# Kernel tuning notes

Measured on AMD Instinct MI355X. Metric: run time of the kernel, lower is better.

Reference implementation:

```python
import jax, jax.numpy as jnp
import numpy as np

K = 20          # cfg.K, k-NN neighbors
NEG = 0.2       # LeakyReLU slope
EPS = 1e-5      # BatchNorm eps (eval mode, running mean=0, var=1)
BN_SCALE = np.float32(1.0 / np.sqrt(1.0 + EPS))


def graph_feature(x, k):
    # x: [B, C, N] -> [B, 2C, N, k] (DGCNN get_graph_feature)
    xt = jnp.swapaxes(x, 1, 2)                                  # [B,N,C]
    xx = jnp.sum(xt * xt, axis=-1)                              # [B,N]
    inner = jnp.einsum('bnc,bmc->bnm', xt, xt)
    negdist = 2.0 * inner - xx[:, :, None] - xx[:, None, :]     # -||xi-xj||^2
    _, idx = jax.lax.top_k(negdist, k)                          # [B,N,k]
    feat = jax.vmap(lambda xb, ib: xb[ib])(xt, idx)             # [B,N,k,C]
    center = jnp.broadcast_to(xt[:, :, None, :], feat.shape)
    out = jnp.concatenate([feat - center, center], axis=-1)     # [B,N,k,2C]
    return jnp.transpose(out, (0, 3, 1, 2))


def edge_layer(x, W, b, g, beta):
    # 1x1 Conv2d + BN(eval) + LeakyReLU + max over k
    f = graph_feature(x, K)                                     # [B,2C,N,k]
    y = jnp.einsum('oc,bcnk->bonk', W, f) + b[:, None, None]
    y = y * (g[:, None, None] * BN_SCALE) + beta[:, None, None]
    y = jnp.where(y >= 0, y, NEG * y)
    return jnp.max(y, axis=-1)                                  # [B,O,N]


def edge_conv(x, Ws, bs, gs, betas):
    for W, b, g, beta in zip(Ws, bs, gs, betas):
        x = edge_layer(x, W, b, g, beta)
    return x


def mha(x, Wi, bi, Wo, bo, nh=8):
    # torch nn.MultiheadAttention(64, 8, batch_first=True), self-attention
    B, N, E = x.shape
    d = E // nh
    qkv = x @ Wi.T + bi
    q, k_, v = jnp.split(qkv, 3, axis=-1)
    hd = lambda t: jnp.transpose(t.reshape(B, N, nh, d), (0, 2, 1, 3))
    q, k_, v = hd(q), hd(k_), hd(v)
    a = jax.nn.softmax(jnp.einsum('bhnd,bhmd->bhnm', q, k_) / np.float32(np.sqrt(d)), axis=-1)
    o = jnp.einsum('bhnm,bhmd->bhnd', a, v)
    o = jnp.transpose(o, (0, 2, 1, 3)).reshape(B, N, E)
    return o @ Wo.T + bo


def branch(feats, cW, cb, cg, cB, sW, sb, sg, sB, Wi, bi, Wo, bo):
    xyz = feats[:, 0:3, :]
    sem = feats[:, 3:, :]
    xyz = edge_conv(xyz, cW, cb, cg, cB)                         # [B,32,N]
    sem = edge_conv(sem, sW, sb, sg, sB)                         # [B,32,N]
    fuse = jnp.concatenate([jnp.swapaxes(xyz, 1, 2), jnp.swapaxes(sem, 1, 2)], axis=2)  # [B,N,64]
    fuse = mha(fuse, Wi, bi, Wo, bo)
    B, N, E = fuse.shape
    return fuse.reshape(B, N, E // 2, 2).mean(axis=-1)           # AvgPool1d(2,2) -> [B,N,32]


def attention_pool(emb, W):
    # SimGNN-style attention readout
    g = jnp.tanh(jnp.mean(emb @ W, axis=1))                      # [B,F]
    scores = jax.nn.sigmoid(jnp.einsum('bnf,bf->bn', emb, g))    # [B,N]
    pooled = jnp.einsum('bnf,bn->bf', emb, scores)               # [B,F]
    return pooled, scores[..., None]


def setup_inputs() -> dict:
    key = jax.random.key(0)
    ks = iter(jax.random.split(key, 48))
    nrm = lambda shape, s=0.05: jax.random.normal(next(ks), shape, dtype=jnp.float32) * s
    B, N = 8, 1024
    inp = {
        'features_1': jax.random.normal(next(ks), (B, 15, N), jnp.float32),
        'features_2': jax.random.normal(next(ks), (B, 15, N), jnp.float32),
    }
    dims_c = [(64, 6), (128, 128), (32, 256)]    # center_conv (in=3)
    dims_s = [(64, 24), (128, 128), (32, 256)]   # sem_conv (in=12)
    for pre, dims in (('c', dims_c), ('s', dims_s)):
        for i, (o, c) in enumerate(dims):
            inp[pre + 'w%d' % i] = nrm((o, c))
            inp[pre + 'b%d' % i] = jnp.zeros((o,), jnp.float32)
            inp[pre + 'g%d' % i] = jnp.ones((o,), jnp.float32)
            inp[pre + 'B%d' % i] = jnp.zeros((o,), jnp.float32)
    inp['mha_wi'] = nrm((192, 64)); inp['mha_bi'] = jnp.zeros((192,), jnp.float32)
    inp['mha_wo'] = nrm((64, 64));  inp['mha_bo'] = jnp.zeros((64,), jnp.float32)
    inp['att_w'] = nrm((32, 32), 0.1)
    inp['ntn_w'] = nrm((32, 32, 16)); inp['ntn_v'] = nrm((16, 32)); inp['ntn_b'] = jnp.zeros((16,), jnp.float32)
    inp['fc1_w'] = nrm((16, 16)); inp['fc1_b'] = jnp.zeros((16,), jnp.float32)
    inp['sc_w'] = nrm((1, 16));  inp['sc_b'] = jnp.zeros((1,), jnp.float32)
    return inp


def reference(features_1, features_2,
              cw0, cb0, cg0, cB0, cw1, cb1, cg1, cB1, cw2, cb2, cg2, cB2,
              sw0, sb0, sg0, sB0, sw1, sb1, sg1, sB1, sw2, sb2, sg2, sB2,
              mha_wi, mha_bi, mha_wo, mha_bo,
              att_w, ntn_w, ntn_v, ntn_b, fc1_w, fc1_b, sc_w, sc_b):
    cW, cb, cg, cB = [cw0, cw1, cw2], [cb0, cb1, cb2], [cg0, cg1, cg2], [cB0, cB1, cB2]
    sW, sb, sg, sB = [sw0, sw1, sw2], [sb0, sb1, sb2], [sg0, sg1, sg2], [sB0, sB1, sB2]
    a1 = branch(features_1, cW, cb, cg, cB, sW, sb, sg, sB, mha_wi, mha_bi, mha_wo, mha_bo)
    a2 = branch(features_2, cW, cb, cg, cB, sW, sb, sg, sB, mha_wi, mha_bi, mha_wo, mha_bo)
    p1, s1 = attention_pool(a1, att_w)
    p2, s2 = attention_pool(a2, att_w)
    d = p1 - p2                                                  # [B,32]
    t = jax.nn.relu(jnp.einsum('bf,fgt,bg->bt', d, ntn_w, d) + d @ ntn_v.T + ntn_b)  # [B,16]
    h = jax.nn.relu(t @ fc1_w.T + fc1_b)
    score = jax.nn.sigmoid(h @ sc_w.T + sc_b).reshape(-1)        # [B]
    return score, s1, s2
```

## Files before the change

### kernel.cpp

```cpp
#include <hip/hip_runtime.h>
#include <math.h>

#define BD 16
#define ND 1024
#define KNN 20
#define NEGS 0.2f
#define BNSC 0.99999500003749969482f
#define KSL 8
#define KPS 128

__device__ __forceinline__ float leakyf(float y){ return y >= 0.f ? y : NEGS*y; }

__device__ __forceinline__ void gl_lds16(const float* g, float* l){
  __builtin_amdgcn_global_load_lds(
      (const __attribute__((address_space(1))) void*)g,
      (__attribute__((address_space(3))) void*)l, 16, 0, 0);
}


template<int C, int CS>
__global__ __launch_bounds__(256) void k_prep(const float* __restrict__ f1,
                                              const float* __restrict__ f2,
                                              float* __restrict__ x,
                                              float* __restrict__ xx, int c0){
  int blk = blockIdx.x;
  int b = blk & 15;
  int n = (blk >> 4)*256 + threadIdx.x;
  const float* feat = (b & 8) ? f2 : f1;
  int b8 = b & 7;
  float v[CS];
  float s = 0.f;
  #pragma unroll
  for (int c = 0; c < C; ++c){
    v[c] = feat[((size_t)(b8*15) + c0 + c)*ND + n];
    s = fmaf(v[c], v[c], s);
  }
  #pragma unroll
  for (int c = C; c < CS; ++c) v[c] = 0.f;
  #pragma unroll
  for (int g = 0; g < CS/4; ++g)
    *(float4*)&x[(size_t)(b*CS + g*4)*ND + (size_t)n*4] =
        make_float4(v[g*4], v[g*4+1], v[g*4+2], v[g*4+3]);
  xx[b*ND + n] = s;
}

__global__ __launch_bounds__(256)
void k_knn(const float* __restrict__ x,
    const float* __restrict__ xx, int* __restrict__ idxp, int CS, int nchunk){
  __shared__ __align__(16) float Xc[2][2][4096];
  int b = blockIdx.x & 15;
  int r0 = (blockIdx.x >> 4)*16;
  int t = threadIdx.x;
  int lane = t & 63;
  int w = __builtin_amdgcn_readfirstlane(t >> 6);
  const float* xb = x + (size_t)b*ND*CS;
  float acc[4][16];
  #pragma unroll
  for (int j = 0; j < 4; ++j)
    #pragma unroll
    for (int q = 0; q < 16; ++q) acc[j][q] = 0.f;

  auto stage = [&](int buf, int ch){
    int g0 = 2*ch, g1 = 2*ch + 1;
    bool v1 = (g1*4 < CS);
    #pragma unroll
    for (int i = 0; i < 4; ++i){
      int m = i*256 + t;
      unsigned ub = (unsigned)((i*256 + (w << 6))*4);
      gl_lds16(&xb[((size_t)g0*ND + m)*4], &Xc[buf][0][ub]);
      if (v1) gl_lds16(&xb[((size_t)g1*ND + m)*4], &Xc[buf][1][ub]);
      else    *(float4*)&Xc[buf][1][m*4] = make_float4(0.f,0.f,0.f,0.f);
    }
  };

  stage(0, 0);
  __syncthreads();
  int cur = 0;
  for (int ch = 0; ch < nchunk; ++ch){
    bool more = (ch + 1 < nchunk);
    if (more) stage(cur ^ 1, ch + 1);
    float4 rv0[4], rv1[4];
    #pragma unroll
    for (int j = 0; j < 4; ++j){
      rv0[j] = *(const float4*)&Xc[cur][0][(r0 + w*4 + j)*4];
      rv1[j] = *(const float4*)&Xc[cur][1][(r0 + w*4 + j)*4];
    }
    #pragma unroll
    for (int q = 0; q < 16; ++q){
      float4 cv0 = *(const float4*)&Xc[cur][0][(q*64 + lane)*4];
      float4 cv1 = *(const float4*)&Xc[cur][1][(q*64 + lane)*4];
      #pragma unroll
      for (int j = 0; j < 4; ++j){
        float s = acc[j][q];
        s = fmaf(rv0[j].x, cv0.x, s); s = fmaf(rv0[j].y, cv0.y, s);
        s = fmaf(rv0[j].z, cv0.z, s); s = fmaf(rv0[j].w, cv0.w, s);
        s = fmaf(rv1[j].x, cv1.x, s); s = fmaf(rv1[j].y, cv1.y, s);
        s = fmaf(rv1[j].z, cv1.z, s); s = fmaf(rv1[j].w, cv1.w, s);
        acc[j][q] = s;
      }
    }
    if (more){
      __syncthreads();
      cur ^= 1;
    }
  }
  float xxm[16];
  #pragma unroll
  for (int q = 0; q < 16; ++q) xxm[q] = xx[b*ND + q*64 + lane];
  unsigned uk[4][16];
  #pragma unroll
  for (int j = 0; j < 4; ++j){
    float xr = xx[b*ND + r0 + w*4 + j];
    #pragma unroll
    for (int q = 0; q < 16; ++q){
      float f = 2.f*acc[j][q] - xr - xxm[q];
      unsigned bv = __float_as_uint(f);
      uk[j][q] = (bv & 0x80000000u) ? ~bv : (bv | 0x80000000u);
    }
  }
  unsigned pref[4] = {0u, 0u, 0u, 0u};
  unsigned done = 0u;
  #pragma unroll 1
  for (int bit = 30; bit >= 0; --bit){
    #pragma unroll
    for (int u = 0; u < 4; ++u){
      if (done & (1u << u)) continue;
      unsigned cand = pref[u] | (1u << bit);
      int c = 0;
      #pragma unroll
      for (int q = 0; q < 16; ++q)
        c += (int)__popcll(__ballot(uk[u][q] >= cand));
      if (c >= KNN){
        pref[u] = cand;
        if (c == KNN) done |= (1u << u);
      }
    }
    if (done == 15u) break;
  }
  unsigned long long mlt = (1ull << lane) - 1ull;
  #pragma unroll
  for (int u = 0; u < 4; ++u){
    unsigned T = pref[u];
    int cg = 0;
    #pragma unroll
    for (int q = 0; q < 16; ++q) cg += (int)__popcll(__ballot(uk[u][q] > T));
    int need_eq = KNN - cg;
    int* op = &idxp[((size_t)(b*ND + r0 + w*4 + u))*KNN];
    int run_gt = 0, run_eq = 0;
    #pragma unroll
    for (int q = 0; q < 16; ++q){
      unsigned k = uk[u][q];
      unsigned long long bg = __ballot(k > T);
      unsigned long long be = __ballot(k == T);
      if (k > T) op[run_gt + (int)__popcll(bg & mlt)] = q*64 + lane;
      if (k == T){
        int r = run_eq + (int)__popcll(be & mlt);
        if (r < need_eq) op[cg + r] = q*64 + lane;
      }
      run_gt += (int)__popcll(bg);
      run_eq += (int)__popcll(be);
    }
  }
}

template<int O>
__global__ __launch_bounds__(256) void k_phaseA(const float* __restrict__ x,
    const float* __restrict__ W, const float* __restrict__ bias,
    const float* __restrict__ gamma, const float* __restrict__ beta,
    float* __restrict__ zs, float* __restrict__ ccv, int C, int XS){
  constexpr int TO = O/16;
  constexpr int WP = O + 4;
  __shared__ float W1s[32*WP];
  __shared__ float dWs[32*WP];
  __shared__ float Xs[32*33];
  int blk = blockIdx.x;
  int b = blk & 15, n0 = (blk >> 4)*32;
  int t = threadIdx.x;
  int ot = t & 15, nt = t >> 4;
  int obase = ot*TO;
  int nl = nt*2;
  float az[TO][2] = {}, ac[TO][2] = {};
  for (int cc = 0; cc < C; cc += 32){
    int KC = (C - cc < 32) ? (C - cc) : 32;
    int NG = (KC + 3) >> 2;
    for (int i = t; i < O*KC; i += 256){
      int o = i % O, c = i / O;
      float w1 = W[(size_t)o*2*C + cc + c];
      float w2 = W[(size_t)o*2*C + C + cc + c];
      W1s[c*WP + o] = w1;
      dWs[c*WP + o] = w2 - w1;
    }
    for (int i = t; i < 32*NG; i += 256){
      int row = i & 31, g = i >> 5;
      float4 v = *(const float4*)&x[(size_t)(b*XS + cc + g*4)*ND + (size_t)(n0+row)*4];
      Xs[(g*4+0)*33 + row] = v.x;
      Xs[(g*4+1)*33 + row] = v.y;
      Xs[(g*4+2)*33 + row] = v.z;
      Xs[(g*4+3)*33 + row] = v.w;
    }
    __syncthreads();
    for (int c = 0; c < KC; ++c){
      float xv0 = Xs[c*33 + nl];
      float xv1 = Xs[c*33 + nl + 1];
      #pragma unroll
      for (int i = 0; i < TO; ++i){
        float w1 = W1s[c*WP + obase + i];
        float dw = dWs[c*WP + obase + i];
        az[i][0] = fmaf(w1, xv0, az[i][0]);
        az[i][1] = fmaf(w1, xv1, az[i][1]);
        ac[i][0] = fmaf(dw, xv0, ac[i][0]);
        ac[i][1] = fmaf(dw, xv1, ac[i][1]);
      }
    }
    __syncthreads();
  }
  #pragma unroll
  for (int i = 0; i < TO; ++i){
    int o = obase + i;
    float alpha = gamma[o]*BNSC;
    float bb = bias[o], be = beta[o];
    #pragma unroll
    for (int q = 0; q < 2; ++q){
      int n = n0 + nl + q;
      size_t off = ((size_t)b*ND + n)*O + o;
      zs[off]  = az[i][q]*alpha;
      ccv[off] = fmaf(ac[i][q] + bb, alpha, be);
    }
  }
}

template<bool DOXX, bool TILED>
__global__ __launch_bounds__(256) void k_phaseB(const float* __restrict__ zs,
    const float* __restrict__ ccv, const int* __restrict__ idxp,
    float* __restrict__ outp, float* __restrict__ xxout,
    int O, int ostride, int ooff){
  int t = threadIdx.x;
  int lane = t & 63, w = t >> 6;
  int b = blockIdx.x & 15;
  int n = (blockIdx.x >> 4)*4 + w;
  int gn = (b << 10) + n;
  int mm[KNN];
  const int* ip = idxp + (size_t)gn*KNN;
  #pragma unroll
  for (int k = 0; k < KNN; ++k) mm[k] = ip[k];
  float sq = 0.f;
  for (int o = lane; o < O; o += 64){
    float cvv = ccv[(size_t)gn*O + o];
    float mx = -INFINITY;
    #pragma unroll 4
    for (int k = 0; k < KNN; ++k){
      float v = leakyf(zs[((size_t)(b*ND) + mm[k])*O + o] + cvv);
      mx = fmaxf(mx, v);
    }
    if (TILED)
      outp[(size_t)(b*O + (o & ~3))*ND + (size_t)n*4 + (o & 3)] = mx;
    else
      outp[(size_t)gn*ostride + ooff + o] = mx;
    if (DOXX) sq = fmaf(mx, mx, sq);
  }
  if (DOXX){
    #pragma unroll
    for (int off = 32; off; off >>= 1) sq += __shfl_down(sq, off);
    if (lane == 0) xxout[gn] = sq;
  }
}

__global__ __launch_bounds__(256) void k_lin(const float* __restrict__ in,
    const float* __restrict__ Wm, const float* __restrict__ bias,
    float* __restrict__ outp){
  int b = blockIdx.x & 15;
  int inner = (blockIdx.x >> 4)*256 + threadIdx.x;
  int o = inner % 192; int n = inner / 192;
  int bn = (b << 10) + n;
  const float4* ip = (const float4*)(in + (size_t)bn*64);
  const float4* wp = (const float4*)(Wm + (size_t)o*64);
  float s = bias[o];
  #pragma unroll
  for (int c = 0; c < 16; ++c){
    float4 a = ip[c], wv = wp[c];
    s = fmaf(a.x, wv.x, s); s = fmaf(a.y, wv.y, s);
    s = fmaf(a.z, wv.z, s); s = fmaf(a.w, wv.w, s);
  }
  outp[(size_t)bn*192 + o] = s;
}

__global__ __launch_bounds__(256, 1) void k_attn_part(const float* __restrict__ qkv,
    float* __restrict__ pl, float* __restrict__ pacc){
  __shared__ __align__(16) float Ks[2][KPS*8];
  __shared__ __align__(16) float Vs[2][KPS*8];
  int blk = blockIdx.x;
  int b = blk & 15; int ksl = (blk >> 4) & 7; int hp = blk >> 7;
  int t = threadIdx.x;
  int hh = t >> 7;
  int h = hp*2 + hh;
  int lq = t & 127;
  for (int i = t; i < 2*KPS*8; i += 256){
    int hi = (i >= KPS*8) ? 1 : 0;
    int r = i - hi*KPS*8;
    int m = r >> 3, dd = r & 7;
    size_t base = ((size_t)b*ND + ksl*KPS + m)*192 + (hp*2 + hi)*8 + dd;
    Ks[hi][r] = qkv[base + 64];
    Vs[hi][r] = qkv[base + 128];
  }
  __syncthreads();
  const float scale = 0.35355339059327373f;
  float q[8][8];
  #pragma unroll
  for (int u = 0; u < 8; ++u){
    int n = u*128 + lq;
    const float4* qp = (const float4*)(qkv + ((size_t)b*ND + n)*192 + h*8);
    float4 q0 = qp[0], q1 = qp[1];
    q[u][0]=q0.x*scale; q[u][1]=q0.y*scale; q[u][2]=q0.z*scale; q[u][3]=q0.w*scale;
    q[u][4]=q1.x*scale; q[u][5]=q1.y*scale; q[u][6]=q1.z*scale; q[u][7]=q1.w*scale;
  }
  float l[8] = {};
  float acc[8][8] = {};
  for (int m = 0; m < KPS; ++m){
    float4 k0 = *(const float4*)&Ks[hh][m*8];
    float4 k1 = *(const float4*)&Ks[hh][m*8+4];
    float4 v0 = *(const float4*)&Vs[hh][m*8];
    float4 v1 = *(const float4*)&Vs[hh][m*8+4];
    #pragma unroll
    for (int u = 0; u < 8; ++u){
      float s;
      s = q[u][0]*k0.x;           s = fmaf(q[u][1], k0.y, s);
      s = fmaf(q[u][2], k0.z, s); s = fmaf(q[u][3], k0.w, s);
      s = fmaf(q[u][4], k1.x, s); s = fmaf(q[u][5], k1.y, s);
      s = fmaf(q[u][6], k1.z, s); s = fmaf(q[u][7], k1.w, s);
      float p = __expf(s);
      l[u] += p;
      acc[u][0] = fmaf(p, v0.x, acc[u][0]);
      acc[u][1] = fmaf(p, v0.y, acc[u][1]);
      acc[u][2] = fmaf(p, v0.z, acc[u][2]);
      acc[u][3] = fmaf(p, v0.w, acc[u][3]);
      acc[u][4] = fmaf(p, v1.x, acc[u][4]);
      acc[u][5] = fmaf(p, v1.y, acc[u][5]);
      acc[u][6] = fmaf(p, v1.z, acc[u][6]);
      acc[u][7] = fmaf(p, v1.w, acc[u][7]);
    }
  }
  #pragma unroll
  for (int u = 0; u < 8; ++u){
    int n = u*128 + lq;
    size_t pidx = (((size_t)(b*8 + h))*8 + ksl)*ND + n;
    pl[pidx] = l[u];
    float4* ap = (float4*)&pacc[pidx*8];
    ap[0] = make_float4(acc[u][0], acc[u][1], acc[u][2], acc[u][3]);
    ap[1] = make_float4(acc[u][4], acc[u][5], acc[u][6], acc[u][7]);
  }
}

__global__ __launch_bounds__(256) void k_attn_comb(const float* __restrict__ pl,
    const float* __restrict__ pacc, float* __restrict__ attno){
  int b = blockIdx.x & 15;
  int inner = (blockIdx.x >> 4)*256 + threadIdx.x;
  int h = inner >> 10; int n = inner & 1023;
  int bh = b*8 + h;
  float L = 0.f;
  float o[8] = {};
  #pragma unroll
  for (int s = 0; s < KSL; ++s){
    size_t pidx = ((size_t)bh*8 + s)*ND + n;
    L += pl[pidx];
    const float4* ap = (const float4*)&pacc[pidx*8];
    float4 a0 = ap[0], a1 = ap[1];
    o[0] += a0.x; o[1] += a0.y; o[2] += a0.z; o[3] += a0.w;
    o[4] += a1.x; o[5] += a1.y; o[6] += a1.z; o[7] += a1.w;
  }
  float inv = 1.f/L;
  float4* dst = (float4*)&attno[((size_t)b*ND + n)*64 + h*8];
  dst[0] = make_float4(o[0]*inv, o[1]*inv, o[2]*inv, o[3]*inv);
  dst[1] = make_float4(o[4]*inv, o[5]*inv, o[6]*inv, o[7]*inv);
}

__global__ __launch_bounds__(256) void k_projmean(const float* __restrict__ attno,
    const float* __restrict__ Wo, const float* __restrict__ bo,
    float* __restrict__ emb){
  int b = blockIdx.x & 15;
  int inner = (blockIdx.x >> 4)*256 + threadIdx.x;
  int n = inner >> 5; int f = inner & 31;
  int bn = (b << 10) + n;
  const float4* ip = (const float4*)(attno + (size_t)bn*64);
  int o0 = 2*f, o1 = 2*f + 1;
  const float4* w0 = (const float4*)(Wo + (size_t)o0*64);
  const float4* w1 = (const float4*)(Wo + (size_t)o1*64);
  float s0 = bo[o0], s1 = bo[o1];
  #pragma unroll
  for (int c = 0; c < 16; ++c){
    float4 a = ip[c], u = w0[c], v = w1[c];
    s0 = fmaf(a.x,u.x,s0); s0 = fmaf(a.y,u.y,s0); s0 = fmaf(a.z,u.z,s0); s0 = fmaf(a.w,u.w,s0);
    s1 = fmaf(a.x,v.x,s1); s1 = fmaf(a.y,v.y,s1); s1 = fmaf(a.z,v.z,s1); s1 = fmaf(a.w,v.w,s1);
  }
  emb[(size_t)bn*32 + f] = 0.5f*(s0 + s1);
}

__global__ __launch_bounds__(256) void k_poolfuse(const float* __restrict__ emb,
    const float* __restrict__ attw, float* __restrict__ sout,
    float* __restrict__ pooled){
  __shared__ float part[8][32];
  __shared__ float meanv[32];
  __shared__ float gv[32];
  __shared__ float sc[ND];
  int b = blockIdx.x, t = threadIdx.x;
  int f = t & 31, j = t >> 5;
  const float* eb = emb + (size_t)b*ND*32;
  float s = 0.f;
  for (int n = j; n < ND; n += 8) s += eb[n*32 + f];
  part[j][f] = s;
  __syncthreads();
  if (t < 32){
    float m = 0.f;
    for (int j2 = 0; j2 < 8; ++j2) m += part[j2][t];
    meanv[t] = m * (1.f/ND);
  }
  __syncthreads();
  if (t < 32){
    float acc = 0.f;
    for (int f2 = 0; f2 < 32; ++f2) acc = fmaf(meanv[f2], attw[f2*32 + t], acc);
    gv[t] = tanhf(acc);
  }
  __syncthreads();
  for (int n = t; n < ND; n += 256){
    const float4* ep = (const float4*)(eb + n*32);
    float acc = 0.f;
    #pragma unroll
    for (int f4 = 0; f4 < 8; ++f4){
      float4 e = ep[f4];
      acc = fmaf(e.x, gv[f4*4+0], acc);
      acc = fmaf(e.y, gv[f4*4+1], acc);
      acc = fmaf(e.z, gv[f4*4+2], acc);
      acc = fmaf(e.w, gv[f4*4+3], acc);
    }
    float sg = 1.f/(1.f + __expf(-acc));
    sout[(size_t)b*ND + n] = sg;
    sc[n] = sg;
  }
  __syncthreads();
  float pacc = 0.f;
  for (int n = j; n < ND; n += 8) pacc = fmaf(eb[n*32 + f], sc[n], pacc);
  part[j][f] = pacc;
  __syncthreads();
  if (t < 32){
    float m = 0.f;
    for (int j2 = 0; j2 < 8; ++j2) m += part[j2][t];
    pooled[b*32 + t] = m;
  }
}

__global__ __launch_bounds__(256) void k_head(const float* __restrict__ p1,
    const float* __restrict__ p2, const float* __restrict__ ntnw,
    const float* __restrict__ ntnv, const float* __restrict__ ntnb,
    const float* __restrict__ fc1w, const float* __restrict__ fc1b,
    const float* __restrict__ scw, const float* __restrict__ scb,
    float* __restrict__ outscore){
  __shared__ __align__(16) float Wl[8192];
  __shared__ float Vl[512];
  __shared__ float F1[256];
  __shared__ float ds[8][32];
  __shared__ float tv[8][16];
  __shared__ float hv[8][16];
  int t = threadIdx.x;
  {
    int b = t >> 5, f = t & 31;
    ds[b][f] = p1[b*32+f] - p2[b*32+f];
  }
  for (int i = t; i < 512; i += 256) Vl[i] = ntnv[i];
  if (t < 256) F1[t] = fc1w[t];
  float acc = 0.f;
  for (int ph = 0; ph < 2; ++ph){
    __syncthreads();
    {
      const float4* src = (const float4*)(ntnw + ph*8192);
      float4* dst = (float4*)Wl;
      for (int i = t; i < 2048; i += 256) dst[i] = src[i];
    }
    __syncthreads();
    if (t < 128){
      int b = t >> 4, tt = t & 15;
      for (int fi = 0; fi < 16; ++fi){
        float df = ds[b][ph*16 + fi];
        #pragma unroll 8
        for (int gg = 0; gg < 32; ++gg)
          acc = fmaf(df*ds[b][gg], Wl[(fi*32+gg)*16 + tt], acc);
      }
    }
  }
  if (t < 128){
    int b = t >> 4, tt = t & 15;
    acc += ntnb[tt];
    for (int gg = 0; gg < 32; ++gg) acc = fmaf(ds[b][gg], Vl[tt*32+gg], acc);
    tv[b][tt] = fmaxf(acc, 0.f);
  }
  __syncthreads();
  if (t < 128){
    int b = t >> 4, i = t & 15;
    float a2 = fc1b[i];
    for (int kk = 0; kk < 16; ++kk) a2 = fmaf(tv[b][kk], F1[i*16+kk], a2);
    hv[b][i] = fmaxf(a2, 0.f);
  }
  __syncthreads();
  if (t < 8){
    float a3 = scb[0];
    for (int i = 0; i < 16; ++i) a3 = fmaf(hv[t][i], scw[i], a3);
    outscore[t] = 1.f/(1.f + __expf(-a3));
  }
}

extern "C" void kernel_launch(void* const* d_in, const int* in_sizes, int n_in,
                              void* d_out, int out_size, void* d_ws, size_t ws_size,
                              hipStream_t stream) {
  auto F = [&](int i){ return (const float*)d_in[i]; };
  const float* f1 = F(0); const float* f2 = F(1);
  const float* cw[3] = { F(2), F(6), F(10) };
  const float* cb[3] = { F(3), F(7), F(11) };
  const float* cg[3] = { F(4), F(8), F(12) };
  const float* cB[3] = { F(5), F(9), F(13) };
  const float* sw[3] = { F(14), F(18), F(22) };
  const float* sb[3] = { F(15), F(19), F(23) };
  const float* sg[3] = { F(16), F(20), F(24) };
  const float* sB[3] = { F(17), F(21), F(25) };
  const float* mha_wi = F(26); const float* mha_bi = F(27);
  const float* mha_wo = F(28); const float* mha_bo = F(29);
  const float* att_w  = F(30);
  const float* ntn_w  = F(31); const float* ntn_v = F(32); const float* ntn_b = F(33);
  const float* fc1_w  = F(34); const float* fc1_b = F(35);
  const float* sc_w   = F(36); const float* sc_b  = F(37);
  float* out = (float*)d_out;

  char* ws = (char*)d_ws;
  const size_t MB = 1 << 20;
  float* xA   = (float*)(ws + 0*MB);
  float* xB   = (float*)(ws + 8*MB);
  float* zs   = (float*)(ws + 16*MB);
  float* cvb  = (float*)(ws + 24*MB);
  int*   idxb = (int*)  (ws + 32*MB);
  float* xxb  = (float*)(ws + 34*MB);
  float* fuse = (float*)(ws + 35*MB);
  float* qkv   = (float*)(ws + 0*MB);
  float* plb   = (float*)(ws + 12*MB);
  float* paccb = (float*)(ws + 16*MB);
  float* attno = (float*)(ws + 48*MB);
  float* emb   = (float*)(ws + 52*MB);
  float* pooled= (float*)(ws + 54*MB);
  (void)ws_size;

  auto knn = [&](const float* xin, int CS, int nch8){
    k_knn<<<BD*64, 256, 0, stream>>>(xin, xxb, idxb, CS, nch8);
  };
  auto phA = [&](const float* xin, int C, int XS, int O, const float* W, const float* bb,
                 const float* gg, const float* be){
    if (O == 64)       k_phaseA<64> <<<BD*32, 256, 0, stream>>>(xin, W, bb, gg, be, zs, cvb, C, XS);
    else if (O == 128) k_phaseA<128><<<BD*32, 256, 0, stream>>>(xin, W, bb, gg, be, zs, cvb, C, XS);
    else               k_phaseA<32> <<<BD*32, 256, 0, stream>>>(xin, W, bb, gg, be, zs, cvb, C, XS);
  };

  for (int part = 0; part < 2; ++part){
    const float* const* Wl = part ? sw : cw;
    const float* const* bl = part ? sb : cb;
    const float* const* gl = part ? sg : cg;
    const float* const* Bl = part ? sB : cB;
    int C0 = part ? 12 : 3;
    int CS0 = part ? 12 : 4;
    if (part) k_prep<12,12><<<BD*ND/256, 256, 0, stream>>>(f1, f2, xA, xxb, 3);
    else      k_prep<3, 4> <<<BD*ND/256, 256, 0, stream>>>(f1, f2, xA, xxb, 0);
    knn(xA, CS0, part ? 2 : 1);
    phA(xA, C0, CS0, 64, Wl[0], bl[0], gl[0], Bl[0]);
    k_phaseB<true,true><<<BD*ND/4, 256, 0, stream>>>(zs, cvb, idxb, xB, xxb, 64, 0, 0);
    knn(xB, 64, 8);
    phA(xB, 64, 64, 128, Wl[1], bl[1], gl[1], Bl[1]);
    k_phaseB<true,true><<<BD*ND/4, 256, 0, stream>>>(zs, cvb, idxb, xA, xxb, 128, 0, 0);
    knn(xA, 128, 16);
    phA(xA, 128, 128, 32, Wl[2], bl[2], gl[2], Bl[2]);
    k_phaseB<false,false><<<BD*ND/4, 256, 0, stream>>>(zs, cvb, idxb, fuse, nullptr, 32, 64, part*32);
  }
  k_lin<<<(BD*ND*192)/256, 256, 0, stream>>>(fuse, mha_wi, mha_bi, qkv);
  k_attn_part<<<BD*4*KSL, 256, 0, stream>>>(qkv, plb, paccb);
  k_attn_comb<<<(BD*8*ND)/256, 256, 0, stream>>>(plb, paccb, attno);
  k_projmean<<<(BD*ND*32)/256, 256, 0, stream>>>(attno, mha_wo, mha_bo, emb);
  k_poolfuse<<<BD, 256, 0, stream>>>(emb, att_w, out + 8, pooled);
  k_head<<<1, 256, 0, stream>>>(pooled, pooled + 256, ntn_w, ntn_v, ntn_b,
                                fc1_w, fc1_b, sc_w, sc_b, out);
}
```

Baseline: 1.103 ms.

## Register-tile the QKV input projection with LDS-staged weights and inputs

Rewrites k_lin as a tiled GEMM. Each block stages the full transposed 192x64 weight matrix and a 32-row input tile in LDS, and each thread computes a 12x2 output micro-tile with float4 stores. This replaces one-output-per-thread dot products that reread input and weights from global memory. In exchange, every block reloads about 48KB of weights, which raises LDS usage, lowers occupancy, and adds bank conflicts on the transposed weight writes.

```diff
diff --git a/kernel.cpp b/kernel.cpp
--- a/kernel.cpp
+++ b/kernel.cpp
@@ -268,20 +268,52 @@
 __global__ __launch_bounds__(256) void k_lin(const float* __restrict__ in,
     const float* __restrict__ Wm, const float* __restrict__ bias,
     float* __restrict__ outp){
-  int b = blockIdx.x & 15;
-  int inner = (blockIdx.x >> 4)*256 + threadIdx.x;
-  int o = inner % 192; int n = inner / 192;
-  int bn = (b << 10) + n;
-  const float4* ip = (const float4*)(in + (size_t)bn*64);
-  const float4* wp = (const float4*)(Wm + (size_t)o*64);
-  float s = bias[o];
-  #pragma unroll
-  for (int c = 0; c < 16; ++c){
-    float4 a = ip[c], wv = wp[c];
-    s = fmaf(a.x, wv.x, s); s = fmaf(a.y, wv.y, s);
-    s = fmaf(a.z, wv.z, s); s = fmaf(a.w, wv.w, s);
-  }
-  outp[(size_t)bn*192 + o] = s;
+  __shared__ float Ws[64*196];
+  __shared__ float Xs[64*33];
+  int blk = blockIdx.x;
+  int b = blk & 15, n0 = (blk >> 4)*32;
+  int bn0 = (b << 10) + n0;
+  int t = threadIdx.x;
+  int ot = t & 15, nt = t >> 4;
+  int obase = ot*12;
+  int nl = nt*2;
+  for (int i = t; i < 192*64; i += 256){
+    int c = i & 63, o = i >> 6;
+    Ws[c*196 + o] = Wm[i];
+  }
+  for (int i = t; i < 32*16; i += 256){
+    int row = i >> 4, c4 = i & 15;
+    float4 v = *(const float4*)&in[((size_t)(bn0 + row))*64 + c4*4];
+    Xs[(c4*4+0)*33 + row] = v.x;
+    Xs[(c4*4+1)*33 + row] = v.y;
+    Xs[(c4*4+2)*33 + row] = v.z;
+    Xs[(c4*4+3)*33 + row] = v.w;
+  }
+  __syncthreads();
+  float acc[12][2];
+  #pragma unroll
+  for (int i = 0; i < 12; ++i){
+    float bb = bias[obase + i];
+    acc[i][0] = bb; acc[i][1] = bb;
+  }
+  for (int c = 0; c < 64; ++c){
+    float xv0 = Xs[c*33 + nl];
+    float xv1 = Xs[c*33 + nl + 1];
+    #pragma unroll
+    for (int i = 0; i < 12; ++i){
+      float wv = Ws[c*196 + obase + i];
+      acc[i][0] = fmaf(wv, xv0, acc[i][0]);
+      acc[i][1] = fmaf(wv, xv1, acc[i][1]);
+    }
+  }
+  #pragma unroll
+  for (int q = 0; q < 2; ++q){
+    float* op = &outp[(size_t)(bn0 + nl + q)*192 + obase];
+    #pragma unroll
+    for (int v4 = 0; v4 < 3; ++v4)
+      *(float4*)&op[v4*4] = make_float4(acc[v4*4+0][q], acc[v4*4+1][q],
+                                        acc[v4*4+2][q], acc[v4*4+3][q]);
+  }
 }
 
 __global__ __launch_bounds__(256, 1) void k_attn_part(const float* __restrict__ qkv,
@@ -573,7 +605,7 @@
     phA(xA, 128, 128, 32, Wl[2], bl[2], gl[2], Bl[2]);
     k_phaseB<false,false><<<BD*ND/4, 256, 0, stream>>>(zs, cvb, idxb, fuse, nullptr, 32, 64, part*32);
   }
-  k_lin<<<(BD*ND*192)/256, 256, 0, stream>>>(fuse, mha_wi, mha_bi, qkv);
+  k_lin<<<BD*32, 256, 0, stream>>>(fuse, mha_wi, mha_bi, qkv);
   k_attn_part<<<BD*4*KSL, 256, 0, stream>>>(qkv, plb, paccb);
   k_attn_comb<<<(BD*8*ND)/256, 256, 0, stream>>>(plb, paccb, attno);
   k_projmean<<<(BD*ND*32)/256, 256, 0, stream>>>(attno, mha_wo, mha_bo, emb);
```

Result: faster. 998.0 us (median of 2 runs) (-9.5%).
